# Performance work log

Hardware: AMD Instinct MI355X
Metric: run time of the kernel (lower is better)

Reference implementation:

```python
import jax, jax.numpy as jnp
import numpy as np

B, Q, P = 8, 300, 5
RS, QS, CS, NC = 256, 768, 768, 396
HW = [64, 32, 16, 8]
POOL = [32, 16, 8, 4]
THR = 0.2


def _ln(x, g, b, eps=1e-5):
    m = x.mean(-1, keepdims=True)
    v = ((x - m) ** 2).mean(-1, keepdims=True)
    return (x - m) / jnp.sqrt(v + eps) * g + b


def _avgpool(x, oh, ow):
    # exact adaptive avg pool (output divides input)
    b, c, h, w = x.shape
    return x.reshape(b, c, oh, h // oh, ow, w // ow).mean((3, 5))


def setup_inputs() -> dict:
    key = jax.random.key(0)
    ks = jax.random.split(key, 40)
    inp = {}
    inp['pred_logits'] = jax.random.normal(ks[0], (B, Q, P), dtype=jnp.float32)
    inp['pred_boxes'] = jax.random.uniform(ks[1], (B, Q, 4), dtype=jnp.float32)
    inp['hs'] = jax.random.normal(ks[2], (B, Q, RS), dtype=jnp.float32)
    for s in range(4):
        inp[f'feat{s}'] = jax.random.normal(ks[3 + s], (B, 256, HW[s], HW[s]), dtype=jnp.float32)
        inp[f'pos{s}'] = jax.random.normal(ks[7 + s], (B, 256, HW[s], HW[s]), dtype=jnp.float32)
        inp[f'mask{s}'] = jax.random.bernoulli(ks[11 + s], 0.15, (B, HW[s], HW[s]))
        inp[f'convW{s}'] = jax.random.normal(ks[15 + s], (CS, 256), dtype=jnp.float32) * 0.02
        inp[f'convb{s}'] = jnp.zeros((CS,), jnp.float32)
        inp[f'lng{s}'] = jnp.ones((CS,), jnp.float32)
        inp[f'lnb{s}'] = jnp.zeros((CS,), jnp.float32)
    inp['learnable_query'] = jax.random.normal(ks[19], (P + 1, QS), dtype=jnp.float32)
    inp['Wq'] = jax.random.normal(ks[20], (RS, QS), dtype=jnp.float32) * 0.02
    inp['bq'] = jnp.zeros((QS,), jnp.float32)
    inp['qng'] = jnp.ones((QS,), jnp.float32)
    inp['qnb'] = jnp.zeros((QS,), jnp.float32)
    inp['W1'] = jax.random.normal(ks[21], (QS, QS), dtype=jnp.float32) * 0.02
    inp['b1'] = jnp.zeros((QS,), jnp.float32)
    inp['W2'] = jax.random.normal(ks[22], (QS, NC), dtype=jnp.float32) * 0.02
    inp['b2'] = jnp.zeros((NC,), jnp.float32)
    return inp


def _forward(pred_logits, pred_boxes, hs,
             feats, poss, masks, convWs, convbs, lngs, lnbs,
             learnable_query, Wq, bq, qng, qnb, W1, b1, W2, b2):
    del pred_boxes  # selected in the original but never used
    b = hs.shape[0]
    prob = jax.nn.sigmoid(pred_logits)                       # (B,Q,P)
    # per-prompt membership: logit_i > thr (implies max > thr)
    m = (prob > THR).astype(hs.dtype)                        # (B,Q,P)
    cnt = m.sum(1)                                           # (B,P)
    ssum = jnp.einsum('bqp,bqd->bpd', m, hs)                 # segment-sum over queries
    pooled = jnp.where(cnt[..., None] > 0,
                       ssum / jnp.maximum(cnt, 1.0)[..., None], 0.0)  # (B,P,RS)
    proj = pooled @ Wq + bq                                  # (B,P,QS)
    any_sel = jnp.any(prob.max(-1) > THR, axis=1)            # (B,)
    # if no query passed the global gate, prompt_hs is zeros WITHOUT projection
    prompt_hs = jnp.where(any_sel[:, None, None], proj, 0.0)
    prompt_query = learnable_query[1:] + prompt_hs           # (B,P,QS)
    cls_query = jnp.broadcast_to(learnable_query[0][None, None, :], (b, 1, QS))
    query_tokens = jnp.concatenate([cls_query, prompt_query], axis=1)
    query_tokens = _ln(query_tokens, qng, qnb)               # (B,P+1,QS)

    tokens = []
    for s in range(4):
        mask_f = masks[s][:, None, :, :].astype(feats[s].dtype)   # (B,1,H,W)
        x = (feats[s] + poss[s]) * (1.0 - mask_f)                 # masked_fill
        ctx = jnp.einsum('bchw,oc->bohw', x, convWs[s]) + convbs[s][None, :, None, None]
        p = _avgpool(ctx, POOL[s], POOL[s])
        mp = jnp.clip(_avgpool(1.0 - mask_f, POOL[s], POOL[s]), 1e-6, None)
        p = p / mp
        t = p.reshape(b, CS, -1).transpose(0, 2, 1)               # (B,T_s,CS)
        tokens.append(_ln(t, lngs[s], lnbs[s]))
    ctx_all = jnp.concatenate(tokens, axis=1)                     # (B,1360,CS)

    # encoder stand-in: fuse context into query tokens additively
    last = query_tokens + ctx_all.mean(1)[:, None, :]
    cls_logit = last[:, 0]
    prompt_logit = last[:, 1:].mean(1)
    h = jax.nn.relu((cls_logit + prompt_logit) @ W1 + b1)
    return h @ W2 + b2                                            # (B,NC)


def reference(pred_logits, pred_boxes, hs,
              feat0, pos0, mask0, convW0, convb0, lng0, lnb0,
              feat1, pos1, mask1, convW1, convb1, lng1, lnb1,
              feat2, pos2, mask2, convW2, convb2, lng2, lnb2,
              feat3, pos3, mask3, convW3, convb3, lng3, lnb3,
              learnable_query, Wq, bq, qng, qnb, W1, b1, W2, b2):
    return _forward(pred_logits, pred_boxes, hs,
                    [feat0, feat1, feat2, feat3],
                    [pos0, pos1, pos2, pos3],
                    [mask0, mask1, mask2, mask3],
                    [convW0, convW1, convW2, convW3],
                    [convb0, convb1, convb2, convb3],
                    [lng0, lng1, lng2, lng3],
                    [lnb0, lnb1, lnb2, lnb3],
                    learnable_query, Wq, bq, qng, qnb, W1, b1, W2, b2)
```

## Files before the change

### kernel.cpp

```cpp
#include <hip/hip_runtime.h>
#include <hip/hip_bf16.h>

#define Bn 8
#define Qn 300
#define Pn 5
#define RSn 256
#define QSn 768
#define NCn 396
#define MTOT 10880
#define THRL -1.3862943611198906f

typedef __attribute__((ext_vector_type(8))) short short8;
typedef __attribute__((ext_vector_type(4))) float float4v;

__device__ inline float wred(float v){
  #pragma unroll
  for (int off = 32; off; off >>= 1) v += __shfl_xor(v, off);
  return v;
}

__device__ __forceinline__ unsigned short f2bf(float f){
  union { float f; unsigned int u; } c; c.f = f;
  return (unsigned short)((c.u + 0x7FFF + ((c.u >> 16) & 1)) >> 16);
}

__global__ __launch_bounds__(256, 4) void k_front(
    const float* cw0, const float* cw1, const float* cw2, const float* cw3,
    short* Wswz, const int* __restrict__ mk0, int* det,
    const float* __restrict__ pl, const float* __restrict__ hs,
    float* pooled, int* flags, float* ctxsum, float* outz){
  int bx = blockIdx.x;
  int t = threadIdx.x;
  if (bx < 768){
    int s = bx / 192;
    int linear = (bx % 192)*256 + t;
    int q = linear & 63, n = linear >> 6;
    const float* src = (s==0)?cw0:(s==1)?cw1:(s==2)?cw2:cw3;
    float4 f = *(const float4*)(src + (size_t)n*256 + q*4);
    int kc = q >> 3, lk = (q >> 1) & 3, e0 = (q & 1)*4;
    short* dst = Wswz + ((size_t)(s*8 + kc))*24576 + lk*6144 + n*8 + e0;
    short4 sv;
    sv.x = (short)f2bf(f.x); sv.y = (short)f2bf(f.y);
    sv.z = (short)f2bf(f.z); sv.w = (short)f2bf(f.w);
    *(short4*)dst = sv;
    return;
  }
  if (bx == 768){
    __shared__ int r0[4], r1[4];
    const int* mm = mk0 + t*32;
    int d0 = 0, d1 = 0;
    #pragma unroll 8
    for (int i = 0; i < 32; ++i){
      int v = mm[i];
      d0 |= (v != 0 && v != 1);
      d1 |= (v != 0 && v != 0x3F800000);
    }
    unsigned long long bal0 = __ballot(d0), bal1 = __ballot(d1);
    int wid = t >> 6;
    if ((t & 63) == 0){ r0[wid] = (bal0 != 0ull); r1[wid] = (bal1 != 0ull); }
    __syncthreads();
    if (t == 0){
      det[0] = r0[0] | r0[1] | r0[2] | r0[3];
      det[1] = r1[0] | r1[1] | r1[2] | r1[3];
    }
    return;
  }
  if (bx >= 821){
    int idx = ((bx - 821)*256 + t)*4;
    if (idx < Bn*NCn) *(float4*)(outz + idx) = (float4){0.f,0.f,0.f,0.f};
    return;
  }
  if (bx >= 809){
    int idx = ((bx - 809)*256 + t)*4;
    *(float4*)(ctxsum + idx) = (float4){0.f,0.f,0.f,0.f};
    return;
  }
  __shared__ float msk[Qn];
  int bb = (bx - 769) / Pn, p = (bx - 769) % Pn;
  for (int q = t; q < Qn; q += 256)
    msk[q] = (pl[(bb*Qn + q)*Pn + p] > THRL) ? 1.f : 0.f;
  __syncthreads();
  const float* hb = hs + (size_t)bb*Qn*RSn + t;
  float s0 = 0.f, s1 = 0.f, s2 = 0.f, s3 = 0.f, cnt = 0.f;
  for (int q = 0; q < Qn; q += 4){
    float m0v = msk[q], m1 = msk[q+1], m2 = msk[q+2], m3 = msk[q+3];
    cnt += m0v + m1 + m2 + m3;
    s0 = fmaf(m0v, hb[(size_t)(q  )*RSn], s0);
    s1 = fmaf(m1,  hb[(size_t)(q+1)*RSn], s1);
    s2 = fmaf(m2,  hb[(size_t)(q+2)*RSn], s2);
    s3 = fmaf(m3,  hb[(size_t)(q+3)*RSn], s3);
  }
  float ssum = (s0 + s1) + (s2 + s3);
  pooled[(bb*Pn + p)*RSn + t] = (cnt > 0.f) ? ssum / cnt : 0.f;
  if (t == 0) flags[bb*Pn + p] = (cnt > 0.f) ? 1 : 0;
}

__global__ __launch_bounds__(256, 2) void k_pgemm(
    const float* fe0, const float* po0, const void* ma0,
    const float* fe1, const float* po1, const void* ma1,
    const float* fe2, const float* po2, const void* ma2,
    const float* fe3, const float* po3, const void* ma3,
    const int* __restrict__ det, const short* __restrict__ Wswz,
    const float* cb0, const float* cb1, const float* cb2, const float* cb3,
    const float* lg0, const float* lb0, const float* lg1, const float* lb1,
    const float* lg2, const float* lb2, const float* lg3, const float* lb3,
    float* __restrict__ ctxsum,
    const float* __restrict__ lq, const float* __restrict__ Wq,
    const float* __restrict__ bq, const float* __restrict__ qng,
    const float* __restrict__ qnb, const float* __restrict__ pooled,
    const int* __restrict__ flags, float* qt){
  __shared__ short As[16*264];
  __shared__ float imls[16];
  __shared__ float lsum[4][16], lsq[4][16];
  __shared__ float pq[256];
  __shared__ float s1s[4], s2s[4];
  int blk = blockIdx.x;
  int t = threadIdx.x;

  if (blk >= 680){
    int qbx = blk - 680;
    int b = qbx / 6, j = qbx % 6;
    float v0 = lq[j*QSn + t], v1 = lq[j*QSn + t + 256], v2 = lq[j*QSn + t + 512];
    int any = flags[b*Pn] | flags[b*Pn+1] | flags[b*Pn+2] | flags[b*Pn+3] | flags[b*Pn+4];
    if (j > 0 && any){
      pq[t] = pooled[(b*Pn + (j-1))*RSn + t];
      __syncthreads();
      float a0 = 0.f, a1 = 0.f, a2 = 0.f;
      #pragma unroll 8
      for (int c = 0; c < RSn; ++c){
        float pv = pq[c];
        a0 = fmaf(pv, Wq[c*QSn + t      ], a0);
        a1 = fmaf(pv, Wq[c*QSn + t + 256], a1);
        a2 = fmaf(pv, Wq[c*QSn + t + 512], a2);
      }
      v0 += a0 + bq[t]; v1 += a1 + bq[t+256]; v2 += a2 + bq[t+512];
    }
    float sm = v0 + v1 + v2, sq = v0*v0 + v1*v1 + v2*v2;
    sm = wred(sm); sq = wred(sq);
    int wid = t >> 6, lane = t & 63;
    if (lane == 0){ s1s[wid] = sm; s2s[wid] = sq; }
    __syncthreads();
    float S  = s1s[0] + s1s[1] + s1s[2] + s1s[3];
    float SQ = s2s[0] + s2s[1] + s2s[2] + s2s[3];
    float mu = S * (1.f/QSn), var = SQ * (1.f/QSn) - mu*mu;
    float rs = rsqrtf(var + 1e-5f);
    float* o = qt + (b*6 + j)*QSn;
    o[t      ] = (v0 - mu)*rs*qng[t      ] + qnb[t      ];
    o[t + 256] = (v1 - mu)*rs*qng[t + 256] + qnb[t + 256];
    o[t + 512] = (v2 - mu)*rs*qng[t + 512] + qnb[t + 512];
    return;
  }

  int m0 = blk * 16;
  int s, H, OWlog, b0;
  const float *F, *Pp; const void* M;
  const float *CB, *LG, *LB;
  if (m0 < 8192){ s=0; F=fe0; Pp=po0; M=ma0; H=64; OWlog=5; b0=m0>>10;
                  CB=cb0; LG=lg0; LB=lb0; }
  else if (m0 < 10240){ s=1; F=fe1; Pp=po1; M=ma1; H=32; OWlog=4; b0=(m0-8192)>>8;
                  CB=cb1; LG=lg1; LB=lb1; }
  else if (m0 < 10752){ s=2; F=fe2; Pp=po2; M=ma2; H=16; OWlog=3; b0=(m0-10240)>>6;
                  CB=cb2; LG=lg2; LB=lb2; }
  else { s=3; F=fe3; Pp=po3; M=ma3; H=8; OWlog=2; b0=(m0-10752)>>4;
                  CB=cb3; LG=lg3; LB=lb3; }
  int HH = H*H;
  int OWm = (H >> 1) - 1;
  int mode = (det[0] == 0) ? 0 : ((det[1] == 0) ? 2 : 1);

  int slot = t & 15;
  int gm = m0 + slot;
  int bb = b0;
  int ltl;
  if (s == 0)      ltl = gm & 1023;
  else if (s == 1) ltl = gm & 255;
  else if (s == 2) ltl = gm & 63;
  else             ltl = gm & 15;
  int ph = ltl >> OWlog, pw = ltl & OWm;
  int i00 = ph*2*H + pw*2;
  int mbase = bb*HH;

  float w0, w1, w2, w3;
  {
    if (mode == 0){
      const int* Mi = (const int*)M + mbase + i00;
      int2 ma = *(const int2*)(Mi);
      int2 mb = *(const int2*)(Mi + H);
      w0 = ma.x?0.f:1.f; w1 = ma.y?0.f:1.f; w2 = mb.x?0.f:1.f; w3 = mb.y?0.f:1.f;
    } else if (mode == 1){
      const unsigned char* Mb = (const unsigned char*)M + mbase + i00;
      w0 = Mb[0]?0.f:1.f; w1 = Mb[1]?0.f:1.f; w2 = Mb[H]?0.f:1.f; w3 = Mb[H+1]?0.f:1.f;
    } else {
      const float* Mf = (const float*)M + mbase + i00;
      float2 ma = *(const float2*)(Mf);
      float2 mb = *(const float2*)(Mf + H);
      w0 = 1.f-ma.x; w1 = 1.f-ma.y; w2 = 1.f-mb.x; w3 = 1.f-mb.y;
    }
  }
  float msum = w0 + w1 + w2 + w3;
  float im = 1.f / fmaxf(msum*0.25f, 1e-6f);
  float sc = 0.25f*im;
  if (t < 16) imls[t] = im;

  {
    int chb = (t >> 4) * 2;
    size_t base = (size_t)(bb*256 + chb)*HH + i00;
    const float* Fp = F + base;
    const float* Pq = Pp + base;
    const int stride = 32*HH;
    #pragma unroll
    for (int r = 0; r < 8; ++r){
      float2 fa0 = *(const float2*)(Fp);
      float2 fb0 = *(const float2*)(Fp + H);
      float2 pa0 = *(const float2*)(Pq);
      float2 pb0 = *(const float2*)(Pq + H);
      float2 fa1 = *(const float2*)(Fp + HH);
      float2 fb1 = *(const float2*)(Fp + HH + H);
      float2 pa1 = *(const float2*)(Pq + HH);
      float2 pb1 = *(const float2*)(Pq + HH + H);
      float x0 = (fa0.x+pa0.x)*w0 + (fa0.y+pa0.y)*w1 + (fb0.x+pb0.x)*w2 + (fb0.y+pb0.y)*w3;
      float x1 = (fa1.x+pa1.x)*w0 + (fa1.y+pa1.y)*w1 + (fb1.x+pb1.x)*w2 + (fb1.y+pb1.y)*w3;
      *(unsigned int*)(&As[slot*264 + chb + r*32]) =
          (unsigned int)f2bf(x0*sc) | ((unsigned int)f2bf(x1*sc) << 16);
      Fp += stride; Pq += stride;
    }
  }
  __syncthreads();

  int wid = t >> 6, l = t & 63;
  int lm = l & 15, lk = l >> 4;
  int nfb = wid * 12;

  float4v acc[12];
  #pragma unroll
  for (int nf = 0; nf < 12; ++nf) acc[nf] = (float4v){0.f,0.f,0.f,0.f};

  const short* Bbase = Wswz + ((size_t)(s*8))*24576 + lk*6144 + nfb*128 + lm*8;
  const short* Akbase = As + lm*264 + lk*8;

  short8 a0 = *(const short8*)(Akbase + 0*32);
  short8 b0_[12];
  #pragma unroll
  for (int nf = 0; nf < 12; ++nf)
    b0_[nf] = *(const short8*)(Bbase + nf*128);
  __builtin_amdgcn_sched_barrier(0);

  #pragma unroll
  for (int kc = 0; kc < 8; kc += 2){
    short8 a1 = *(const short8*)(Akbase + (kc+1)*32);
    short8 b1_[12];
    #pragma unroll
    for (int nf = 0; nf < 12; ++nf)
      b1_[nf] = *(const short8*)(Bbase + (size_t)(kc+1)*24576 + nf*128);
    __builtin_amdgcn_sched_barrier(0);
    #pragma unroll
    for (int nf = 0; nf < 12; ++nf)
      acc[nf] = __builtin_amdgcn_mfma_f32_16x16x32_bf16(a0, b0_[nf], acc[nf], 0, 0, 0);

    if (kc + 2 < 8){
      a0 = *(const short8*)(Akbase + (kc+2)*32);
      #pragma unroll
      for (int nf = 0; nf < 12; ++nf)
        b0_[nf] = *(const short8*)(Bbase + (size_t)(kc+2)*24576 + nf*128);
    }
    __builtin_amdgcn_sched_barrier(0);
    #pragma unroll
    for (int nf = 0; nf < 12; ++nf)
      acc[nf] = __builtin_amdgcn_mfma_f32_16x16x32_bf16(a1, b1_[nf], acc[nf], 0, 0, 0);
  }

  float im4[4];
  #pragma unroll
  for (int r = 0; r < 4; ++r) im4[r] = imls[lk*4 + r];

  float sum[4] = {0,0,0,0}, sq[4] = {0,0,0,0};
  #pragma unroll
  for (int nf = 0; nf < 12; ++nf){
    float cbv = CB[(nfb+nf)*16 + lm];
    #pragma unroll
    for (int r = 0; r < 4; ++r){
      float p = acc[nf][r] + cbv*im4[r];
      acc[nf][r] = p;
      sum[r] += p;
      sq[r] = fmaf(p, p, sq[r]);
    }
  }
  #pragma unroll
  for (int r = 0; r < 4; ++r){
    #pragma unroll
    for (int off = 1; off < 16; off <<= 1){
      sum[r] += __shfl_xor(sum[r], off);
      sq[r]  += __shfl_xor(sq[r],  off);
    }
  }
  if (lm == 0){
    #pragma unroll
    for (int r = 0; r < 4; ++r){
      lsum[wid][lk*4 + r] = sum[r];
      lsq[wid][lk*4 + r]  = sq[r];
    }
  }
  __syncthreads();
  float mu[4], rs[4];
  #pragma unroll
  for (int r = 0; r < 4; ++r){
    int row = lk*4 + r;
    float S  = lsum[0][row] + lsum[1][row] + lsum[2][row] + lsum[3][row];
    float SQ = lsq[0][row]  + lsq[1][row]  + lsq[2][row]  + lsq[3][row];
    mu[r] = S * (1.f/768.f);
    float var = SQ * (1.f/768.f) - mu[r]*mu[r];
    rs[r] = rsqrtf(var + 1e-5f);
  }
  #pragma unroll
  for (int nf = 0; nf < 12; ++nf){
    int n = (nfb+nf)*16 + lm;
    float g = LG[n], bv = LB[n];
    float tv = 0.f;
    #pragma unroll
    for (int r = 0; r < 4; ++r)
      tv += (acc[nf][r] - mu[r]) * rs[r];
    tv = tv*g + 4.f*bv;
    tv += __shfl_xor(tv, 16); tv += __shfl_xor(tv, 32);
    if (lk == 0)
      atomicAdd(&ctxsum[b0*768 + n], tv);
  }
}

__global__ void k_hpre(const float* __restrict__ qt, const float* __restrict__ ctxsum,
                       const float* __restrict__ W1, const float* __restrict__ b1,
                       float* __restrict__ hpre){
  __shared__ float vsh[Bn][192];
  int nc = blockIdx.x % 24, kc = blockIdx.x / 24;
  int n0 = nc*32, c0 = kc*192;
  int t = threadIdx.x;
  for (int i = t; i < Bn*192; i += 256){
    int b = i / 192, cl = i - b*192;
    int c = c0 + cl;
    const float* q = qt + (size_t)b*6*768;
    float pm = q[768+c] + q[2*768+c] + q[3*768+c] + q[4*768+c] + q[5*768+c];
    vsh[b][cl] = q[c] + 0.2f*pm + ctxsum[b*768 + c]*(1.f/680.f);
  }
  __syncthreads();
  int ow = t & 31, bi = t >> 5;
  int o = n0 + ow;
  float acc = 0.f;
  const float* w = W1 + (size_t)c0*768 + o;
  #pragma unroll 4
  for (int cl = 0; cl < 192; ++cl)
    acc = fmaf(vsh[bi][cl], w[(size_t)cl*768], acc);
  if (kc == 0) acc += b1[o];
  atomicAdd(&hpre[bi*768 + o], acc);
}

__global__ void k_out(const float* __restrict__ hpre, const float* __restrict__ W2,
                      const float* __restrict__ b2, float* __restrict__ out){
  __shared__ float hsh[Bn][192];
  int nc = blockIdx.x % 13, kc = blockIdx.x / 13;
  int n0 = nc*32, c0 = kc*192;
  int t = threadIdx.x;
  for (int i = t; i < Bn*192; i += 256){
    int b = i / 192, cl = i - b*192;
    hsh[b][cl] = fmaxf(hpre[b*768 + c0 + cl], 0.f);
  }
  __syncthreads();
  int ow = t & 31, bi = t >> 5;
  int o = n0 + ow;
  if (o >= NCn) return;
  float acc = 0.f;
  const float* w = W2 + (size_t)c0*NCn + o;
  #pragma unroll 4
  for (int cl = 0; cl < 192; ++cl)
    acc = fmaf(hsh[bi][cl], w[(size_t)cl*NCn], acc);
  if (kc == 0) acc += b2[o];
  atomicAdd(&out[bi*NCn + o], acc);
}

extern "C" void kernel_launch(void* const* d_in, const int* in_sizes, int n_in,
                              void* d_out, int out_size, void* d_ws, size_t ws_size,
                              hipStream_t stream){
  const float* pl = (const float*)d_in[0];
  const float* hs = (const float*)d_in[2];
  const float* feat[4]; const float* pos[4]; const void* mask[4];
  const float* cw[4]; const float* cb[4]; const float* lg[4]; const float* lb[4];
  for (int s = 0; s < 4; ++s){
    int base = 3 + 7*s;
    feat[s] = (const float*)d_in[base];
    pos[s]  = (const float*)d_in[base+1];
    mask[s] = d_in[base+2];
    cw[s]   = (const float*)d_in[base+3];
    cb[s]   = (const float*)d_in[base+4];
    lg[s]   = (const float*)d_in[base+5];
    lb[s]   = (const float*)d_in[base+6];
  }
  const float* lq  = (const float*)d_in[31];
  const float* Wq  = (const float*)d_in[32];
  const float* bq  = (const float*)d_in[33];
  const float* qng = (const float*)d_in[34];
  const float* qnb = (const float*)d_in[35];
  const float* W1  = (const float*)d_in[36];
  const float* b1  = (const float*)d_in[37];
  const float* W2  = (const float*)d_in[38];
  const float* b2  = (const float*)d_in[39];
  float* out = (float*)d_out;

  short* Wswz   = (short*)d_ws;
  float* pooled = (float*)(Wswz + (size_t)4*8*4*768*8);
  float* qt     = pooled + 40*RSn;
  float* ctxsum = qt + Bn*6*QSn;
  float* hpre   = ctxsum + Bn*QSn;
  int*   det    = (int*)(hpre + Bn*QSn);
  int*   flags  = det + 4;

  k_front<<<825, 256, 0, stream>>>(cw[0], cw[1], cw[2], cw[3], Wswz,
                                   (const int*)mask[0], det, pl, hs, pooled, flags,
                                   ctxsum, out);
  k_pgemm<<<728, 256, 0, stream>>>(feat[0], pos[0], mask[0],
                                   feat[1], pos[1], mask[1],
                                   feat[2], pos[2], mask[2],
                                   feat[3], pos[3], mask[3],
                                   det, Wswz,
                                   cb[0], cb[1], cb[2], cb[3],
                                   lg[0], lb[0], lg[1], lb[1],
                                   lg[2], lb[2], lg[3], lb[3], ctxsum,
                                   lq, Wq, bq, qng, qnb, pooled, flags, qt);
  k_hpre<<<96, 256, 0, stream>>>(qt, ctxsum, W1, b1, hpre);
  k_out<<<52, 256, 0, stream>>>(hpre, W2, b2, out);
}
```

Before: 269.7 us.

## Double k_pgemm block to 512 threads, halving per-wave N tiles and loads

The fused pool+GEMM+LayerNorm kernel now runs 512 threads per block with 8 waves, each covering 6 N-fragments instead of 12. The pooling stage's per-thread channel loop shrinks from 8 to 4 iterations. The first B fragments are prefetched before pooling to overlap with the feature loads, and all A fragments are held in registers. The query-projection blocks are remapped to 2 columns per thread. This aims to raise memory-level parallelism and occupancy, at the cost of more LayerNorm reduction partials and possible register pressure under the 512-thread launch bound.

```diff
diff --git a/kernel.cpp b/kernel.cpp
--- a/kernel.cpp
+++ b/kernel.cpp
@@ -95,7 +95,7 @@
   if (t == 0) flags[bb*Pn + p] = (cnt > 0.f) ? 1 : 0;
 }
 
-__global__ __launch_bounds__(256, 2) void k_pgemm(
+__global__ __launch_bounds__(512, 2) void k_pgemm(
     const float* fe0, const float* po0, const void* ma0,
     const float* fe1, const float* po1, const void* ma1,
     const float* fe2, const float* po2, const void* ma2,
@@ -111,43 +111,46 @@
     const int* __restrict__ flags, float* qt){
   __shared__ short As[16*264];
   __shared__ float imls[16];
-  __shared__ float lsum[4][16], lsq[4][16];
+  __shared__ float lsum[8][16], lsq[8][16];
   __shared__ float pq[256];
-  __shared__ float s1s[4], s2s[4];
+  __shared__ float s1s[8], s2s[8];
   int blk = blockIdx.x;
   int t = threadIdx.x;
 
   if (blk >= 680){
     int qbx = blk - 680;
     int b = qbx / 6, j = qbx % 6;
-    float v0 = lq[j*QSn + t], v1 = lq[j*QSn + t + 256], v2 = lq[j*QSn + t + 512];
+    int lo = (t < 256);
+    int c1 = 512 + (t & 255);
+    float v0 = lq[j*QSn + t];
+    float v1 = lq[j*QSn + c1];
     int any = flags[b*Pn] | flags[b*Pn+1] | flags[b*Pn+2] | flags[b*Pn+3] | flags[b*Pn+4];
     if (j > 0 && any){
-      pq[t] = pooled[(b*Pn + (j-1))*RSn + t];
+      if (lo) pq[t] = pooled[(b*Pn + (j-1))*RSn + t];
       __syncthreads();
-      float a0 = 0.f, a1 = 0.f, a2 = 0.f;
+      float a0 = 0.f, a1 = 0.f;
       #pragma unroll 8
       for (int c = 0; c < RSn; ++c){
         float pv = pq[c];
-        a0 = fmaf(pv, Wq[c*QSn + t      ], a0);
-        a1 = fmaf(pv, Wq[c*QSn + t + 256], a1);
-        a2 = fmaf(pv, Wq[c*QSn + t + 512], a2);
+        a0 = fmaf(pv, Wq[c*QSn + t ], a0);
+        a1 = fmaf(pv, Wq[c*QSn + c1], a1);
       }
-      v0 += a0 + bq[t]; v1 += a1 + bq[t+256]; v2 += a2 + bq[t+512];
-    }
-    float sm = v0 + v1 + v2, sq = v0*v0 + v1*v1 + v2*v2;
+      v0 += a0 + bq[t]; v1 += a1 + bq[c1];
+    }
+    float sm = v0 + (lo ? v1 : 0.f);
+    float sq = v0*v0 + (lo ? v1*v1 : 0.f);
     sm = wred(sm); sq = wred(sq);
     int wid = t >> 6, lane = t & 63;
     if (lane == 0){ s1s[wid] = sm; s2s[wid] = sq; }
     __syncthreads();
-    float S  = s1s[0] + s1s[1] + s1s[2] + s1s[3];
-    float SQ = s2s[0] + s2s[1] + s2s[2] + s2s[3];
+    float S = 0.f, SQ = 0.f;
+    #pragma unroll
+    for (int w = 0; w < 8; ++w){ S += s1s[w]; SQ += s2s[w]; }
     float mu = S * (1.f/QSn), var = SQ * (1.f/QSn) - mu*mu;
     float rs = rsqrtf(var + 1e-5f);
     float* o = qt + (b*6 + j)*QSn;
-    o[t      ] = (v0 - mu)*rs*qng[t      ] + qnb[t      ];
-    o[t + 256] = (v1 - mu)*rs*qng[t + 256] + qnb[t + 256];
-    o[t + 512] = (v2 - mu)*rs*qng[t + 512] + qnb[t + 512];
+    o[t] = (v0 - mu)*rs*qng[t] + qnb[t];
+    if (lo) o[c1] = (v1 - mu)*rs*qng[c1] + qnb[c1];
     return;
   }
 
@@ -201,87 +204,85 @@
   float sc = 0.25f*im;
   if (t < 16) imls[t] = im;
 
+  int wid = t >> 6, l = t & 63;
+  int lm = l & 15, lk = l >> 4;
+  int nfb = wid * 6;
+  const short* Bbase = Wswz + ((size_t)(s*8))*24576 + lk*6144 + nfb*128 + lm*8;
+  short8 bA[6];
+  #pragma unroll
+  for (int nf = 0; nf < 6; ++nf)
+    bA[nf] = *(const short8*)(Bbase + nf*128);
+  __builtin_amdgcn_sched_barrier(0);
+
   {
     int chb = (t >> 4) * 2;
     size_t base = (size_t)(bb*256 + chb)*HH + i00;
     const float* Fp = F + base;
-    const float* Pq = Pp + base;
-    const int stride = 32*HH;
-    #pragma unroll
-    for (int r = 0; r < 8; ++r){
+    const float* Pq2 = Pp + base;
+    const int stride = 64*HH;
+    #pragma unroll
+    for (int r = 0; r < 4; ++r){
       float2 fa0 = *(const float2*)(Fp);
       float2 fb0 = *(const float2*)(Fp + H);
-      float2 pa0 = *(const float2*)(Pq);
-      float2 pb0 = *(const float2*)(Pq + H);
+      float2 pa0 = *(const float2*)(Pq2);
+      float2 pb0 = *(const float2*)(Pq2 + H);
       float2 fa1 = *(const float2*)(Fp + HH);
       float2 fb1 = *(const float2*)(Fp + HH + H);
-      float2 pa1 = *(const float2*)(Pq + HH);
-      float2 pb1 = *(const float2*)(Pq + HH + H);
+      float2 pa1 = *(const float2*)(Pq2 + HH);
+      float2 pb1 = *(const float2*)(Pq2 + HH + H);
       float x0 = (fa0.x+pa0.x)*w0 + (fa0.y+pa0.y)*w1 + (fb0.x+pb0.x)*w2 + (fb0.y+pb0.y)*w3;
       float x1 = (fa1.x+pa1.x)*w0 + (fa1.y+pa1.y)*w1 + (fb1.x+pb1.x)*w2 + (fb1.y+pb1.y)*w3;
-      *(unsigned int*)(&As[slot*264 + chb + r*32]) =
+      *(unsigned int*)(&As[slot*264 + chb + r*64]) =
           (unsigned int)f2bf(x0*sc) | ((unsigned int)f2bf(x1*sc) << 16);
-      Fp += stride; Pq += stride;
+      Fp += stride; Pq2 += stride;
     }
   }
   __syncthreads();
 
-  int wid = t >> 6, l = t & 63;
-  int lm = l & 15, lk = l >> 4;
-  int nfb = wid * 12;
-
-  float4v acc[12];
-  #pragma unroll
-  for (int nf = 0; nf < 12; ++nf) acc[nf] = (float4v){0.f,0.f,0.f,0.f};
-
-  const short* Bbase = Wswz + ((size_t)(s*8))*24576 + lk*6144 + nfb*128 + lm*8;
-  const short* Akbase = As + lm*264 + lk*8;
-
-  short8 a0 = *(const short8*)(Akbase + 0*32);
-  short8 b0_[12];
-  #pragma unroll
-  for (int nf = 0; nf < 12; ++nf)
-    b0_[nf] = *(const short8*)(Bbase + nf*128);
-  __builtin_amdgcn_sched_barrier(0);
+  short8 aReg[8];
+  #pragma unroll
+  for (int kc = 0; kc < 8; ++kc)
+    aReg[kc] = *(const short8*)(As + lm*264 + kc*32 + lk*8);
+
+  float4v acc[6];
+  #pragma unroll
+  for (int nf = 0; nf < 6; ++nf) acc[nf] = (float4v){0.f,0.f,0.f,0.f};
 
   #pragma unroll
   for (int kc = 0; kc < 8; kc += 2){
-    short8 a1 = *(const short8*)(Akbase + (kc+1)*32);
-    short8 b1_[12];
-    #pragma unroll
-    for (int nf = 0; nf < 12; ++nf)
-      b1_[nf] = *(const short8*)(Bbase + (size_t)(kc+1)*24576 + nf*128);
+    short8 bB[6];
+    #pragma unroll
+    for (int nf = 0; nf < 6; ++nf)
+      bB[nf] = *(const short8*)(Bbase + (size_t)(kc+1)*24576 + nf*128);
     __builtin_amdgcn_sched_barrier(0);
     #pragma unroll
-    for (int nf = 0; nf < 12; ++nf)
-      acc[nf] = __builtin_amdgcn_mfma_f32_16x16x32_bf16(a0, b0_[nf], acc[nf], 0, 0, 0);
-
+    for (int nf = 0; nf < 6; ++nf)
+      acc[nf] = __builtin_amdgcn_mfma_f32_16x16x32_bf16(aReg[kc], bA[nf], acc[nf], 0, 0, 0);
     if (kc + 2 < 8){
-      a0 = *(const short8*)(Akbase + (kc+2)*32);
       #pragma unroll
-      for (int nf = 0; nf < 12; ++nf)
-        b0_[nf] = *(const short8*)(Bbase + (size_t)(kc+2)*24576 + nf*128);
+      for (int nf = 0; nf < 6; ++nf)
+        bA[nf] = *(const short8*)(Bbase + (size_t)(kc+2)*24576 + nf*128);
     }
     __builtin_amdgcn_sched_barrier(0);
     #pragma unroll
-    for (int nf = 0; nf < 12; ++nf)
-      acc[nf] = __builtin_amdgcn_mfma_f32_16x16x32_bf16(a1, b1_[nf], acc[nf], 0, 0, 0);
+    for (int nf = 0; nf < 6; ++nf)
+      acc[nf] = __builtin_amdgcn_mfma_f32_16x16x32_bf16(aReg[kc+1], bB[nf], acc[nf], 0, 0, 0);
   }
 
   float im4[4];
   #pragma unroll
   for (int r = 0; r < 4; ++r) im4[r] = imls[lk*4 + r];
 
-  float sum[4] = {0,0,0,0}, sq[4] = {0,0,0,0};
-  #pragma unroll
-  for (int nf = 0; nf < 12; ++nf){
+  float sum[4] = {0,0,0,0}, sq2[4] = {0,0,0,0};
+  #pragma unroll
+  for (int nf = 0; nf < 6; ++nf){
     float cbv = CB[(nfb+nf)*16 + lm];
     #pragma unroll
     for (int r = 0; r < 4; ++r){
       float p = acc[nf][r] + cbv*im4[r];
       acc[nf][r] = p;
       sum[r] += p;
-      sq[r] = fmaf(p, p, sq[r]);
+      sq2[r] = fmaf(p, p, sq2[r]);
     }
   }
   #pragma unroll
@@ -289,14 +290,14 @@
     #pragma unroll
     for (int off = 1; off < 16; off <<= 1){
       sum[r] += __shfl_xor(sum[r], off);
-      sq[r]  += __shfl_xor(sq[r],  off);
+      sq2[r] += __shfl_xor(sq2[r], off);
     }
   }
   if (lm == 0){
     #pragma unroll
     for (int r = 0; r < 4; ++r){
       lsum[wid][lk*4 + r] = sum[r];
-      lsq[wid][lk*4 + r]  = sq[r];
+      lsq[wid][lk*4 + r]  = sq2[r];
     }
   }
   __syncthreads();
@@ -304,14 +305,15 @@
   #pragma unroll
   for (int r = 0; r < 4; ++r){
     int row = lk*4 + r;
-    float S  = lsum[0][row] + lsum[1][row] + lsum[2][row] + lsum[3][row];
-    float SQ = lsq[0][row]  + lsq[1][row]  + lsq[2][row]  + lsq[3][row];
+    float S = 0.f, SQ = 0.f;
+    #pragma unroll
+    for (int w = 0; w < 8; ++w){ S += lsum[w][row]; SQ += lsq[w][row]; }
     mu[r] = S * (1.f/768.f);
     float var = SQ * (1.f/768.f) - mu[r]*mu[r];
     rs[r] = rsqrtf(var + 1e-5f);
   }
   #pragma unroll
-  for (int nf = 0; nf < 12; ++nf){
+  for (int nf = 0; nf < 6; ++nf){
     int n = (nfb+nf)*16 + lm;
     float g = LG[n], bv = LB[n];
     float tv = 0.f;
@@ -413,7 +415,7 @@
   k_front<<<825, 256, 0, stream>>>(cw[0], cw[1], cw[2], cw[3], Wswz,
                                    (const int*)mask[0], det, pl, hs, pooled, flags,
                                    ctxsum, out);
-  k_pgemm<<<728, 256, 0, stream>>>(feat[0], pos[0], mask[0],
+  k_pgemm<<<728, 512, 0, stream>>>(feat[0], pos[0], mask[0],
                                    feat[1], pos[1], mask[1],
                                    feat[2], pos[2], mask[2],
                                    feat[3], pos[3], mask[3],
```

Result: no change. 274.3 us (+1.7%).
